# Optimization experiments

Hardware: AMD Instinct MI355X
Metric: run time of the kernel (lower is better)

The kernel has to match this reference:

```python
import jax, jax.numpy as jnp
import numpy as np

B, N, T = 1, 4096, 512
WQ, HK = 32, 128
ATOM_S, ATOM_Z, TOKEN_S, TOKEN_Z = 128, 16, 384, 128
FEAT = 3 + 1 + 128 + 4 * 64  # 388


def _indexing_matrix(K, Wq, Hk):
    # faithful port of get_indexing_matrix: one-hot banded gather matrix [2K, K*h]
    h = Hk // (Wq // 2)
    ar = jnp.arange(2 * K)
    idx = jnp.clip(ar[None, :] - ar[:, None] + h // 2, 0, h + 1)
    idx = idx.reshape(K, 2, 2 * K)[:, 0, :]                 # [K, 2K]
    oh = jax.nn.one_hot(idx, h + 2, dtype=jnp.float32)[..., 1:-1]  # [K, 2K, h]
    return jnp.transpose(oh, (1, 0, 2)).reshape(2 * K, K * h)


def _to_keys(x, M, Wq, Hk):
    b, n, d = x.shape
    k = n // Wq
    x = x.reshape(b, 2 * k, Wq // 2, d)
    return jnp.einsum('bjid,jk->bkid', x, M).reshape(b, k, Hk, d)


def _ln(x, g, b, eps=1e-5):
    m = jnp.mean(x, axis=-1, keepdims=True)
    v = jnp.var(x, axis=-1, keepdims=True)
    return (x - m) * jax.lax.rsqrt(v + eps) * g + b


def setup_inputs() -> dict:
    key = jax.random.key(0)
    ks = jax.random.split(key, 24)
    s = 0.02
    tok_idx = jnp.sort(jax.random.randint(ks[0], (B, N), 0, T), axis=-1)
    return {
        'ref_pos': jax.random.normal(ks[1], (B, N, 3), jnp.float32),
        'ref_charge': jax.random.normal(ks[2], (B, N), jnp.float32),
        'ref_element': jax.random.uniform(ks[3], (B, N, 128), jnp.float32),
        'ref_atom_name_chars': jax.random.uniform(ks[4], (B, N, 4, 64), jnp.float32),
        'atom_pad_mask': jnp.ones((B, N), dtype=bool),
        'ref_space_uid': jnp.sort(jax.random.randint(ks[5], (B, N), 0, 512), axis=-1),
        'atom_to_token': jax.nn.one_hot(tok_idx, T, dtype=jnp.float32),
        's_trunk': jax.random.normal(ks[6], (B, T, TOKEN_S), jnp.float32),
        'z': jax.random.normal(ks[7], (B, T, T, TOKEN_Z), jnp.float32),
        # learned params, stored [in, out] so y = x @ W (+ b)
        'W_feat': jax.random.normal(ks[8], (FEAT, ATOM_S), jnp.float32) * s,
        'b_feat': jnp.zeros((ATOM_S,), jnp.float32),
        'W_pos': jax.random.normal(ks[9], (3, ATOM_Z), jnp.float32) * s,
        'W_dist': jax.random.normal(ks[10], (1, ATOM_Z), jnp.float32) * s,
        'W_mask': jax.random.normal(ks[11], (1, ATOM_Z), jnp.float32) * s,
        'ln_s_g': jnp.ones((TOKEN_S,), jnp.float32),
        'ln_s_b': jnp.zeros((TOKEN_S,), jnp.float32),
        'W_s2c': jax.random.normal(ks[12], (TOKEN_S, ATOM_S), jnp.float32) * s,
        'ln_z_g': jnp.ones((TOKEN_Z,), jnp.float32),
        'ln_z_b': jnp.zeros((TOKEN_Z,), jnp.float32),
        'W_z2p': jax.random.normal(ks[13], (TOKEN_Z, ATOM_Z), jnp.float32) * s,
        'W_cq': jax.random.normal(ks[14], (ATOM_S, ATOM_Z), jnp.float32) * s,
        'W_ck': jax.random.normal(ks[15], (ATOM_S, ATOM_Z), jnp.float32) * s,
        'W_m1': jax.random.normal(ks[16], (ATOM_Z, ATOM_Z), jnp.float32) * s,
        'W_m2': jax.random.normal(ks[17], (ATOM_Z, ATOM_Z), jnp.float32) * s,
        'W_m3': jax.random.normal(ks[18], (ATOM_Z, ATOM_Z), jnp.float32) * s,
    }


def reference(ref_pos, ref_charge, ref_element, ref_atom_name_chars, atom_pad_mask,
              ref_space_uid, atom_to_token, s_trunk, z,
              W_feat, b_feat, W_pos, W_dist, W_mask,
              ln_s_g, ln_s_b, W_s2c, ln_z_g, ln_z_b, W_z2p,
              W_cq, W_ck, W_m1, W_m2, W_m3):
    b, n, _ = ref_pos.shape
    k = n // WQ
    atom_feats = jnp.concatenate(
        [ref_pos, ref_charge[..., None], ref_element,
         ref_atom_name_chars.reshape(b, n, 4 * 64)], axis=-1)
    c = atom_feats @ W_feat + b_feat                       # [B,N,atom_s]
    q = c
    M = _indexing_matrix(k, WQ, HK)
    tk = lambda x: _to_keys(x, M, WQ, HK)

    pos_q = ref_pos.reshape(b, k, WQ, 1, 3)
    pos_k = tk(ref_pos).reshape(b, k, 1, HK, 3)
    d = pos_k - pos_q                                      # [B,K,W,H,3]
    d_norm = 1.0 / (1.0 + jnp.sum(d * d, axis=-1, keepdims=True))

    mq = atom_pad_mask.reshape(b, k, WQ, 1)
    mk = tk(atom_pad_mask[..., None].astype(jnp.float32)).reshape(b, k, 1, HK) > 0.5
    uq = ref_space_uid.reshape(b, k, WQ, 1)
    uk = tk(ref_space_uid[..., None].astype(jnp.float32)).reshape(b, k, 1, HK).astype(ref_space_uid.dtype)
    v = (mq & mk & (uq == uk)).astype(jnp.float32)[..., None]  # [B,K,W,H,1]

    p = (d @ W_pos) * v
    p = p + (d_norm @ W_dist) * v
    p = p + (v @ W_mask) * v

    # structure_prediction branch
    s2c = _ln(s_trunk, ln_s_g, ln_s_b) @ W_s2c             # [B,T,atom_s]
    c = c + jnp.einsum('bnt,btd->bnd', atom_to_token, s2c)
    a2t_q = atom_to_token.reshape(b, k, WQ, -1)            # [B,K,W,T]
    a2t_k = tk(atom_to_token)                              # [B,K,H,T]
    zp = _ln(z, ln_z_g, ln_z_b) @ W_z2p                    # [B,T,T,atom_z]
    tmp = jnp.einsum('bwki,bijd->bwkjd', a2t_q, zp)        # [B,K,W,T,atom_z]
    p = p + jnp.einsum('bwkjd,bwlj->bwkld', tmp, a2t_k)    # [B,K,W,H,atom_z]

    p = p + jax.nn.relu(c).reshape(b, k, WQ, 1, -1) @ W_cq
    p = p + jax.nn.relu(tk(c)).reshape(b, k, 1, HK, -1) @ W_ck

    h1 = jax.nn.relu(p) @ W_m1
    h2 = jax.nn.relu(h1) @ W_m2
    p = p + jax.nn.relu(h2) @ W_m3
    return (q, c, p)
```

## Files before the change

kernel.cpp:

```cpp
#include <hip/hip_runtime.h>

#define N_ATOMS 4096
#define T_TOK   512
#define TOKEN_S 384
#define TOKEN_Z 128

using bfrag = __attribute__((ext_vector_type(8))) short;
using f4    = __attribute__((ext_vector_type(4))) float;

__device__ __forceinline__ short f2bf(float f) {
    unsigned u = __float_as_uint(f);
    unsigned r = u + 0x7FFFu + ((u >> 16) & 1u);
    return (short)(r >> 16);
}
__device__ __forceinline__ float bf2f(unsigned short s) {
    return __uint_as_float(((unsigned)s) << 16);
}

__global__ __launch_bounds__(256) void setup_kernel(
    const float* __restrict__ a2t, const float* __restrict__ Wz,
    const float* __restrict__ gz, const float* __restrict__ bz,
    const float* __restrict__ Wf, const float* __restrict__ Wcq,
    const float* __restrict__ Wck, const float* __restrict__ Ws2c,
    const float* __restrict__ gs, const float* __restrict__ bs,
    int* __restrict__ tok, short* __restrict__ zpW,
    short* __restrict__ featW, short* __restrict__ WcqF,
    short* __restrict__ WckF, short* __restrict__ s2cW,
    float* __restrict__ bias16, float* __restrict__ cs16,
    float* __restrict__ cs128, float* __restrict__ bs128,
    int* __restrict__ lo, int* __restrict__ hi) {
    const int b = blockIdx.x, tid = threadIdx.x;
    if (b >= 53) {
        const int wave = tid >> 6, lane = tid & 63;
        const int n = (b - 53) * 4 + wave;
        const float* row = a2t + (size_t)n * T_TOK;
        int found = 0;
#pragma unroll
        for (int m = 0; m < T_TOK / 64; ++m)
            if (row[lane + 64 * m] > 0.5f) found = lane + 64 * m;
#pragma unroll
        for (int off = 32; off >= 1; off >>= 1)
            found = max(found, __shfl_xor(found, off, 64));
        if (lane == 0) tok[n] = found;
        return;
    }
    if (b == 51) {
        const int o = tid >> 3, s = tid & 7;
        const float* vec = (o < 16) ? bz : gz;
        const int n = o & 15;
        float p = 0.f;
#pragma unroll
        for (int i = 0; i < 16; ++i) {
            const int k = s + 8 * i;
            p += vec[k] * Wz[k * 16 + n];
        }
        p += __shfl_xor(p, 1, 64); p += __shfl_xor(p, 2, 64);
        p += __shfl_xor(p, 4, 64);
        if (s == 0) { if (o < 16) bias16[n] = p; else cs16[n] = p; }
        return;
    }
    if (b == 52) {
        lo[tid] = 0x7FFFFFFF; lo[tid + 256] = 0x7FFFFFFF;
        hi[tid] = -1;         hi[tid + 256] = -1;
        const int o = tid & 127, arr = tid >> 7;
        const float* vec = arr ? bs : gs;
        float s = 0.f;
        for (int k = 0; k < TOKEN_S; ++k)
            s += vec[k] * Ws2c[(size_t)k * 128 + o];
        if (arr) bs128[o] = s; else cs128[o] = s;
        return;
    }
    const int id = b * 256 + tid;
    const int lane = id & 63, fs = id >> 6;
    const int quad = lane >> 4, n = lane & 15;
    short v[8];
    short* dst;
    if (fs < 4) {
#pragma unroll
        for (int j = 0; j < 8; ++j) {
            int k = fs * 32 + quad * 8 + j;
            v[j] = f2bf(gz[k] * Wz[k * 16 + n]);
        }
        dst = zpW + (size_t)(fs * 64 + lane) * 8;
    } else if (fs < 100) {
        const int idx = fs - 4, kb = idx >> 3, nt = idx & 7;
#pragma unroll
        for (int j = 0; j < 8; ++j) {
            int f = 4 + kb * 32 + quad * 8 + j;
            v[j] = f2bf(Wf[(size_t)f * 128 + nt * 16 + n]);
        }
        dst = featW + (size_t)(idx * 64 + lane) * 8;
    } else if (fs < 104) {
        const int kb = fs - 100;
#pragma unroll
        for (int j = 0; j < 8; ++j) {
            int k = kb * 32 + quad * 8 + j;
            v[j] = f2bf(Wcq[k * 16 + n]);
        }
        dst = WcqF + (size_t)(kb * 64 + lane) * 8;
    } else if (fs < 108) {
        const int kb = fs - 104;
#pragma unroll
        for (int j = 0; j < 8; ++j) {
            int k = kb * 32 + quad * 8 + j;
            v[j] = f2bf(Wck[k * 16 + n]);
        }
        dst = WckF + (size_t)(kb * 64 + lane) * 8;
    } else {
        const int idx = fs - 108, kb = idx >> 3, nt = idx & 7;
#pragma unroll
        for (int j = 0; j < 8; ++j) {
            int k = kb * 32 + quad * 8 + j;
            v[j] = f2bf(gs[k] * Ws2c[(size_t)k * 128 + nt * 16 + n]);
        }
        dst = s2cW + (size_t)(idx * 64 + lane) * 8;
    }
#pragma unroll
    for (int j = 0; j < 8; ++j) dst[j] = v[j];
}

__global__ __launch_bounds__(256) void band_kernel(
    const int* __restrict__ tok, int* __restrict__ lo, int* __restrict__ hi) {
    const int a = blockIdx.x * 256 + threadIdx.x;
    const int t = tok[a];
    int am = a - 79; if (am < 0) am = 0;
    int ap = a + 79; if (ap > N_ATOMS - 1) ap = N_ATOMS - 1;
    atomicMin(&lo[t], tok[am]);
    atomicMax(&hi[t], tok[ap]);
}

__global__ __launch_bounds__(512) void worklist_kernel(
    const int* __restrict__ lo, const int* __restrict__ hi,
    int* __restrict__ wl, int* __restrict__ wl_count) {
    __shared__ int scan[512];
    const int t = threadIdx.x;
    const int l = lo[t], h = hi[t];
    const int n = (h >= l) ? ((h - l) >> 4) + 1 : 0;
    scan[t] = n;
    __syncthreads();
    for (int off = 1; off < 512; off <<= 1) {
        int add = (t >= off) ? scan[t - off] : 0;
        __syncthreads();
        scan[t] += add;
        __syncthreads();
    }
    const int off0 = scan[t] - n;
    for (int i = 0; i < n; ++i) {
        int tk0 = l + i * 16;
        if (tk0 > T_TOK - 16) tk0 = T_TOK - 16;
        wl[off0 + i] = (t << 16) | tk0;
    }
    if (t == 511) *wl_count = scan[511];
}

__global__ __launch_bounds__(256) void s2c_mfma_kernel(
    const float* __restrict__ s_trunk, const short* __restrict__ s2cW,
    const float* __restrict__ cs128, const float* __restrict__ bs128,
    float* __restrict__ s2c) {
    const int wave = threadIdx.x >> 6, lane = threadIdx.x & 63;
    const int m = lane & 15, quad = lane >> 4;
    const int wg = blockIdx.x * 4 + wave;
    const int tile = wg >> 3, nt = wg & 7;
    const int t0 = tile * 16;
    const float* xrow = s_trunk + (size_t)(t0 + m) * TOKEN_S;

    bfrag A[12];
    float xs = 0.f, xq = 0.f;
#pragma unroll
    for (int kb = 0; kb < 12; ++kb) {
        const float4* p = (const float4*)(xrow + kb * 32 + quad * 8);
        float4 x0 = p[0], x1 = p[1];
        const float xv[8] = {x0.x, x0.y, x0.z, x0.w, x1.x, x1.y, x1.z, x1.w};
#pragma unroll
        for (int j = 0; j < 8; ++j) {
            A[kb][j] = f2bf(xv[j]);
            xs += xv[j]; xq = fmaf(xv[j], xv[j], xq);
        }
    }
    xs += __shfl_xor(xs, 16, 64); xs += __shfl_xor(xs, 32, 64);
    xq += __shfl_xor(xq, 16, 64); xq += __shfl_xor(xq, 32, 64);
    const float mean = xs * (1.f / TOKEN_S);
    const float var  = xq * (1.f / TOKEN_S) - mean * mean;
    const float rstd = rsqrtf(var + 1e-5f);
    const float mrs  = mean * rstd;

    const bfrag* Bb = (const bfrag*)s2cW;
    f4 acc = {0.f, 0.f, 0.f, 0.f};
#pragma unroll
    for (int kb = 0; kb < 12; ++kb)
        acc = __builtin_amdgcn_mfma_f32_16x16x32_bf16(
            A[kb], Bb[(kb * 8 + nt) * 64 + lane], acc, 0, 0, 0);

    const int cn = nt * 16 + m;
    const float csn = cs128[cn], bsn = bs128[cn];
#pragma unroll
    for (int reg = 0; reg < 4; ++reg) {
        const int r = quad * 4 + reg;
        const float rs = __shfl(rstd, r, 64);
        const float ms = __shfl(mrs, r, 64);
        s2c[(size_t)(t0 + r) * 128 + cn] = rs * acc[reg] - ms * csn + bsn;
    }
}

__global__ __launch_bounds__(256) void zp_wl_kernel(
    const float* __restrict__ z, const short* __restrict__ zpW,
    const float* __restrict__ bias16, const float* __restrict__ cs16,
    const int* __restrict__ wl, const int* __restrict__ wl_count,
    unsigned short* __restrict__ zp_bf) {
    const int wave = threadIdx.x >> 6, lane = threadIdx.x & 63;
    const int m = lane & 15, quad = lane >> 4;
    const int nwaves = gridDim.x * 4;
    const int count = *wl_count;
    const bfrag* wb = (const bfrag*)zpW;
    const float csn = cs16[m], bn = bias16[m];

    for (int idx = blockIdx.x * 4 + wave; idx < count; idx += nwaves) {
        const int e = wl[idx];
        const int tq = e >> 16, tk0 = e & 0xFFFF;
        const size_t r0 = (size_t)tq * T_TOK + tk0;
        const float* zrow = z + (r0 + m) * (size_t)TOKEN_Z;

        bfrag A[4];
        float xs = 0.f, xq = 0.f;
#pragma unroll
        for (int kb = 0; kb < 4; ++kb) {
            const float4* p = (const float4*)(zrow + kb * 32 + quad * 8);
            float4 x0 = p[0], x1 = p[1];
            const float xv[8] = {x0.x, x0.y, x0.z, x0.w,
                                 x1.x, x1.y, x1.z, x1.w};
#pragma unroll
            for (int j = 0; j < 8; ++j) {
                A[kb][j] = f2bf(xv[j]);
                xs += xv[j]; xq = fmaf(xv[j], xv[j], xq);
            }
        }
        xs += __shfl_xor(xs, 16, 64); xs += __shfl_xor(xs, 32, 64);
        xq += __shfl_xor(xq, 16, 64); xq += __shfl_xor(xq, 32, 64);
        const float mean = xs * (1.f / TOKEN_Z);
        const float var  = xq * (1.f / TOKEN_Z) - mean * mean;
        const float rstd = rsqrtf(var + 1e-5f);
        const float mrs  = mean * rstd;

        f4 acc = {0.f, 0.f, 0.f, 0.f};
#pragma unroll
        for (int kb = 0; kb < 4; ++kb)
            acc = __builtin_amdgcn_mfma_f32_16x16x32_bf16(
                A[kb], wb[kb * 64 + lane], acc, 0, 0, 0);
#pragma unroll
        for (int reg = 0; reg < 4; ++reg) {
            const int r = quad * 4 + reg;
            const float rs = __shfl(rstd, r, 64);
            const float ms = __shfl(mrs, r, 64);
            zp_bf[(r0 + r) * 16 + m] =
                (unsigned short)f2bf(rs * acc[reg] - ms * csn + bn);
        }
    }
}

__global__ __launch_bounds__(128) void featcatk_kernel(
    const float* __restrict__ pos, const float* __restrict__ charge,
    const float* __restrict__ elem, const float* __restrict__ namec,
    const float* __restrict__ Wf, const float* __restrict__ bf,
    const float* __restrict__ s2c, const int* __restrict__ tok,
    const short* __restrict__ featW, const short* __restrict__ WcqF,
    const short* __restrict__ WckF, float* __restrict__ q_out,
    float* __restrict__ c_out, float* __restrict__ acq,
    float* __restrict__ ack) {
    __shared__ short ctile[16 * 136];
    const int wave = threadIdx.x >> 6, lane = threadIdx.x & 63;
    const int m = lane & 15, quad = lane >> 4;
    const int a0 = blockIdx.x * 16;
    const int ntb = wave * 4;

    f4 acc[4];
#pragma unroll
    for (int nt = 0; nt < 4; ++nt) acc[nt] = (f4){0.f, 0.f, 0.f, 0.f};
    const bfrag* Bb = (const bfrag*)featW;
#pragma unroll
    for (int kb = 0; kb < 12; ++kb) {
        const int f0 = kb * 32 + quad * 8;
        const float* src = (kb < 4)
            ? (elem + (size_t)(a0 + m) * 128 + f0)
            : (namec + (size_t)(a0 + m) * 256 + f0 - 128);
        float4 x0 = ((const float4*)src)[0];
        float4 x1 = ((const float4*)src)[1];
        bfrag A;
        A[0] = f2bf(x0.x); A[1] = f2bf(x0.y); A[2] = f2bf(x0.z); A[3] = f2bf(x0.w);
        A[4] = f2bf(x1.x); A[5] = f2bf(x1.y); A[6] = f2bf(x1.z); A[7] = f2bf(x1.w);
#pragma unroll
        for (int nt = 0; nt < 4; ++nt)
            acc[nt] = __builtin_amdgcn_mfma_f32_16x16x32_bf16(
                A, Bb[(kb * 8 + ntb + nt) * 64 + lane], acc[nt], 0, 0, 0);
    }
    float px[4], py[4], pz[4], ch[4];
    int tk4[4];
#pragma unroll
    for (int reg = 0; reg < 4; ++reg) {
        const int a = a0 + quad * 4 + reg;
        px[reg] = pos[a * 3 + 0]; py[reg] = pos[a * 3 + 1];
        pz[reg] = pos[a * 3 + 2]; ch[reg] = charge[a];
        tk4[reg] = tok[a];
    }
#pragma unroll
    for (int nt = 0; nt < 4; ++nt) {
        const int cn = (ntb + nt) * 16 + m;
        const float w0 = Wf[cn], w1 = Wf[128 + cn], w2 = Wf[256 + cn],
                    w3 = Wf[384 + cn], bv = bf[cn];
#pragma unroll
        for (int reg = 0; reg < 4; ++reg) {
            const int r = quad * 4 + reg;
            float qv = acc[nt][reg] + px[reg] * w0 + py[reg] * w1 +
                       pz[reg] * w2 + ch[reg] * w3 + bv;
            q_out[(size_t)(a0 + r) * 128 + cn] = qv;
            float cv = qv + s2c[(size_t)tk4[reg] * 128 + cn];
            c_out[(size_t)(a0 + r) * 128 + cn] = cv;
            ctile[r * 136 + cn] = f2bf(fmaxf(cv, 0.f));
        }
    }
    __syncthreads();
    const bfrag* BW = wave ? (const bfrag*)WckF : (const bfrag*)WcqF;
    float* dst = wave ? ack : acq;
    f4 a2 = {0.f, 0.f, 0.f, 0.f};
#pragma unroll
    for (int kb = 0; kb < 4; ++kb) {
        bfrag Af = *(const bfrag*)&ctile[m * 136 + kb * 32 + quad * 8];
        a2 = __builtin_amdgcn_mfma_f32_16x16x32_bf16(Af, BW[kb * 64 + lane],
                                                     a2, 0, 0, 0);
    }
#pragma unroll
    for (int reg = 0; reg < 4; ++reg)
        dst[(size_t)(a0 + quad * 4 + reg) * 16 + m] = a2[reg];
}

__global__ __launch_bounds__(256) void pair_mfma_kernel(
    const float* __restrict__ pos, const int* __restrict__ uid,
    const int* __restrict__ tok, const unsigned short* __restrict__ zp_bf,
    const float* __restrict__ acq, const float* __restrict__ ack,
    const float* __restrict__ W_pos, const float* __restrict__ W_dist,
    const float* __restrict__ W_mask, const float* __restrict__ W_m1,
    const float* __restrict__ W_m2, const float* __restrict__ W_m3,
    float* __restrict__ p_out) {
    const int wave = threadIdx.x >> 6, lane = threadIdx.x & 63;
    const int m = lane & 15, quad = lane >> 4;
    const int qa = blockIdx.x * 4 + wave;
    const int j = qa >> 5;

    bfrag A1, A2, A3;
#pragma unroll
    for (int jj = 0; jj < 4; ++jj) {
        const int d = quad * 4 + jj;
        A1[jj] = f2bf(W_m1[d * 16 + m]); A1[jj + 4] = 0;
        A2[jj] = f2bf(W_m2[d * 16 + m]); A2[jj + 4] = 0;
        A3[jj] = f2bf(W_m3[d * 16 + m]); A3[jj + 4] = 0;
    }
    float wp0[4], wp1[4], wp2[4], wd[4], wm[4];
#pragma unroll
    for (int jj = 0; jj < 4; ++jj) {
        const int d = quad * 4 + jj;
        wp0[jj] = W_pos[d]; wp1[jj] = W_pos[16 + d]; wp2[jj] = W_pos[32 + d];
        wd[jj] = W_dist[d]; wm[jj] = W_mask[d];
    }
    const float pqx = pos[qa * 3 + 0], pqy = pos[qa * 3 + 1],
                pqz = pos[qa * 3 + 2];
    const int uq = uid[qa], tq = tok[qa];
    const float4 aq = *(const float4*)(acq + (size_t)qa * 16 + quad * 4);
    const float aqv[4] = {aq.x, aq.y, aq.z, aq.w};
    float* pbase = p_out + (size_t)qa * 2048;

    const f4 zero = {0.f, 0.f, 0.f, 0.f};
#pragma unroll
    for (int g = 0; g < 8; ++g) {
        const int kk = g * 16 + m;
        const int src = j * 32 + kk - 48;
        const bool valid = ((unsigned)src < (unsigned)N_ATOMS);
        float dx = 0.f, dy = 0.f, dz = 0.f, dn = 0.f, vflag = 0.f;
        float zv[4] = {0.f, 0.f, 0.f, 0.f}, av[4] = {0.f, 0.f, 0.f, 0.f};
        if (valid) {
            dx = pos[src * 3 + 0] - pqx;
            dy = pos[src * 3 + 1] - pqy;
            dz = pos[src * 3 + 2] - pqz;
            dn = 1.f / (1.f + dx * dx + dy * dy + dz * dz);
            vflag = (uid[src] == uq) ? 1.f : 0.f;
            const int tk_ = tok[src];
            ushort4 zl = *(const ushort4*)(zp_bf +
                            ((size_t)tq * T_TOK + tk_) * 16 + quad * 4);
            float4 al = *(const float4*)(ack + (size_t)src * 16 + quad * 4);
            zv[0] = bf2f(zl.x); zv[1] = bf2f(zl.y);
            zv[2] = bf2f(zl.z); zv[3] = bf2f(zl.w);
            av[0] = al.x; av[1] = al.y; av[2] = al.z; av[3] = al.w;
        }
        float pb[4];
        bfrag B;
#pragma unroll
        for (int jj = 0; jj < 4; ++jj) {
            float t = dx * wp0[jj] + dy * wp1[jj] + dz * wp2[jj] +
                      dn * wd[jj] + wm[jj];
            pb[jj] = vflag * t + zv[jj] + av[jj] + aqv[jj];
            B[jj] = f2bf(fmaxf(pb[jj], 0.f));
            B[jj + 4] = 0;
        }
        f4 t1 = __builtin_amdgcn_mfma_f32_16x16x32_bf16(A1, B, zero, 0, 0, 0);
        bfrag B2;
#pragma unroll
        for (int jj = 0; jj < 4; ++jj) {
            B2[jj] = f2bf(fmaxf(t1[jj], 0.f)); B2[jj + 4] = 0;
        }
        f4 t2 = __builtin_amdgcn_mfma_f32_16x16x32_bf16(A2, B2, zero, 0, 0, 0);
        bfrag B3;
#pragma unroll
        for (int jj = 0; jj < 4; ++jj) {
            B3[jj] = f2bf(fmaxf(t2[jj], 0.f)); B3[jj + 4] = 0;
        }
        f4 t3 = __builtin_amdgcn_mfma_f32_16x16x32_bf16(A3, B3, zero, 0, 0, 0);
        float4 o = make_float4(pb[0] + t3[0], pb[1] + t3[1],
                               pb[2] + t3[2], pb[3] + t3[3]);
        *(float4*)(pbase + kk * 16 + quad * 4) = o;
    }
}

extern "C" void kernel_launch(void* const* d_in, const int* in_sizes, int n_in,
                              void* d_out, int out_size, void* d_ws, size_t ws_size,
                              hipStream_t stream) {
    const float* ref_pos     = (const float*)d_in[0];
    const float* ref_charge  = (const float*)d_in[1];
    const float* ref_element = (const float*)d_in[2];
    const float* ref_name    = (const float*)d_in[3];
    const int*   uid         = (const int*)d_in[5];
    const float* a2t         = (const float*)d_in[6];
    const float* s_trunk     = (const float*)d_in[7];
    const float* z           = (const float*)d_in[8];
    const float* W_feat      = (const float*)d_in[9];
    const float* b_feat      = (const float*)d_in[10];
    const float* W_pos       = (const float*)d_in[11];
    const float* W_dist      = (const float*)d_in[12];
    const float* W_mask      = (const float*)d_in[13];
    const float* ln_s_g      = (const float*)d_in[14];
    const float* ln_s_b      = (const float*)d_in[15];
    const float* W_s2c       = (const float*)d_in[16];
    const float* ln_z_g      = (const float*)d_in[17];
    const float* ln_z_b      = (const float*)d_in[18];
    const float* W_z2p       = (const float*)d_in[19];
    const float* W_cq        = (const float*)d_in[20];
    const float* W_ck        = (const float*)d_in[21];
    const float* W_m1        = (const float*)d_in[22];
    const float* W_m2        = (const float*)d_in[23];
    const float* W_m3        = (const float*)d_in[24];

    float* out = (float*)d_out;
    float* q_out = out;
    float* c_out = out + 524288;
    float* p_out = out + 1048576;

    char* w = (char*)d_ws;
    unsigned short* zp_bf = (unsigned short*)w;
    float* s2c  = (float*)(w + 8388608);
    float* acq  = s2c + 65536;
    float* ack  = acq + 65536;
    int*   tok  = (int*)(ack + 65536);
    short* zpW   = (short*)(tok + 4096);
    short* featW = zpW + 2048;
    short* WcqF  = featW + 49152;
    short* WckF  = WcqF + 2048;
    short* s2cW  = WckF + 2048;
    float* bias16 = (float*)(s2cW + 49152);
    float* cs16   = bias16 + 16;
    float* cs128  = cs16 + 16;
    float* bs128  = cs128 + 128;
    int*   lo     = (int*)(bs128 + 128);
    int*   hi     = lo + 512;
    int*   wl     = hi + 512;
    int*   wl_cnt = wl + 16448;

    setup_kernel<<<1077, 256, 0, stream>>>(a2t, W_z2p, ln_z_g, ln_z_b,
                                           W_feat, W_cq, W_ck, W_s2c,
                                           ln_s_g, ln_s_b, tok, zpW, featW,
                                           WcqF, WckF, s2cW, bias16, cs16,
                                           cs128, bs128, lo, hi);
    band_kernel<<<16, 256, 0, stream>>>(tok, lo, hi);
    worklist_kernel<<<1, 512, 0, stream>>>(lo, hi, wl, wl_cnt);
    s2c_mfma_kernel<<<64, 256, 0, stream>>>(s_trunk, s2cW, cs128, bs128, s2c);
    zp_wl_kernel<<<512, 256, 0, stream>>>(z, zpW, bias16, cs16, wl, wl_cnt,
                                          zp_bf);
    featcatk_kernel<<<256, 128, 0, stream>>>(ref_pos, ref_charge, ref_element,
                                             ref_name, W_feat, b_feat, s2c, tok,
                                             featW, WcqF, WckF,
                                             q_out, c_out, acq, ack);
    pair_mfma_kernel<<<1024, 256, 0, stream>>>(ref_pos, uid, tok, zp_bf,
                                               acq, ack, W_pos, W_dist, W_mask,
                                               W_m1, W_m2, W_m3, p_out);
}
```

Measured before the change: 277.7 us.

## Merge band/worklist into s2c kernel and zp into feat kernel to cut launches

Replaces the separate band (global atomics) and worklist kernels with one extra block of the s2c kernel, which builds lo/hi with shared-memory atomics and scans them locally. The zp worklist kernel and the feature/c kernel become one launch split by block index. Seven launches drop to four, which removes launch gaps and lets independent work share one grid. The cost is heterogeneous blocks: a single serial block handles the banding, and the feature blocks now process 32 atoms with 256 threads.

```diff
diff --git a/kernel.cpp b/kernel.cpp
--- a/kernel.cpp
+++ b/kernel.cpp
@@ -27,8 +27,7 @@
     short* __restrict__ featW, short* __restrict__ WcqF,
     short* __restrict__ WckF, short* __restrict__ s2cW,
     float* __restrict__ bias16, float* __restrict__ cs16,
-    float* __restrict__ cs128, float* __restrict__ bs128,
-    int* __restrict__ lo, int* __restrict__ hi) {
+    float* __restrict__ cs128, float* __restrict__ bs128) {
     const int b = blockIdx.x, tid = threadIdx.x;
     if (b >= 53) {
         const int wave = tid >> 6, lane = tid & 63;
@@ -60,8 +59,6 @@
         return;
     }
     if (b == 52) {
-        lo[tid] = 0x7FFFFFFF; lo[tid + 256] = 0x7FFFFFFF;
-        hi[tid] = -1;         hi[tid + 256] = -1;
         const int o = tid & 127, arr = tid >> 7;
         const float* vec = arr ? bs : gs;
         float s = 0.f;
@@ -119,49 +116,50 @@
     for (int j = 0; j < 8; ++j) dst[j] = v[j];
 }
 
-__global__ __launch_bounds__(256) void band_kernel(
-    const int* __restrict__ tok, int* __restrict__ lo, int* __restrict__ hi) {
-    const int a = blockIdx.x * 256 + threadIdx.x;
-    const int t = tok[a];
-    int am = a - 79; if (am < 0) am = 0;
-    int ap = a + 79; if (ap > N_ATOMS - 1) ap = N_ATOMS - 1;
-    atomicMin(&lo[t], tok[am]);
-    atomicMax(&hi[t], tok[ap]);
-}
-
-__global__ __launch_bounds__(512) void worklist_kernel(
-    const int* __restrict__ lo, const int* __restrict__ hi,
-    int* __restrict__ wl, int* __restrict__ wl_count) {
-    __shared__ int scan[512];
-    const int t = threadIdx.x;
-    const int l = lo[t], h = hi[t];
-    const int n = (h >= l) ? ((h - l) >> 4) + 1 : 0;
-    scan[t] = n;
-    __syncthreads();
-    for (int off = 1; off < 512; off <<= 1) {
-        int add = (t >= off) ? scan[t - off] : 0;
-        __syncthreads();
-        scan[t] += add;
-        __syncthreads();
-    }
-    const int off0 = scan[t] - n;
-    for (int i = 0; i < n; ++i) {
-        int tk0 = l + i * 16;
-        if (tk0 > T_TOK - 16) tk0 = T_TOK - 16;
-        wl[off0 + i] = (t << 16) | tk0;
-    }
-    if (t == 511) *wl_count = scan[511];
-}
-
-__global__ __launch_bounds__(256) void s2c_mfma_kernel(
+__global__ __launch_bounds__(512) void s2c_band_kernel(
     const float* __restrict__ s_trunk, const short* __restrict__ s2cW,
     const float* __restrict__ cs128, const float* __restrict__ bs128,
-    float* __restrict__ s2c) {
+    const int* __restrict__ tok, float* __restrict__ s2c,
+    int* __restrict__ wl, int* __restrict__ wl_count) {
+    __shared__ int sh_lo[512], sh_hi[512], scan[512];
+    const int b = blockIdx.x;
+    if (b == 32) {
+        const int t = threadIdx.x;
+        sh_lo[t] = 0x7FFFFFFF; sh_hi[t] = -1;
+        __syncthreads();
+#pragma unroll
+        for (int i = 0; i < 8; ++i) {
+            const int a = t * 8 + i;
+            const int tt = tok[a];
+            int am = a - 79; if (am < 0) am = 0;
+            int ap = a + 79; if (ap > N_ATOMS - 1) ap = N_ATOMS - 1;
+            atomicMin(&sh_lo[tt], tok[am]);
+            atomicMax(&sh_hi[tt], tok[ap]);
+        }
+        __syncthreads();
+        const int l = sh_lo[t], h = sh_hi[t];
+        const int n = (h >= l) ? ((h - l) >> 4) + 1 : 0;
+        scan[t] = n;
+        __syncthreads();
+        for (int off = 1; off < 512; off <<= 1) {
+            int add = (t >= off) ? scan[t - off] : 0;
+            __syncthreads();
+            scan[t] += add;
+            __syncthreads();
+        }
+        const int off0 = scan[t] - n;
+        for (int i = 0; i < n; ++i) {
+            int tk0 = l + i * 16;
+            if (tk0 > T_TOK - 16) tk0 = T_TOK - 16;
+            wl[off0 + i] = (t << 16) | tk0;
+        }
+        if (t == 511) *wl_count = scan[511];
+        return;
+    }
     const int wave = threadIdx.x >> 6, lane = threadIdx.x & 63;
     const int m = lane & 15, quad = lane >> 4;
-    const int wg = blockIdx.x * 4 + wave;
-    const int tile = wg >> 3, nt = wg & 7;
-    const int t0 = tile * 16;
+    const int nt = wave;
+    const int t0 = b * 16;
     const float* xrow = s_trunk + (size_t)(t0 + m) * TOKEN_S;
 
     bfrag A[12];
@@ -202,62 +200,11 @@
     }
 }
 
-__global__ __launch_bounds__(256) void zp_wl_kernel(
+__global__ __launch_bounds__(256) void zp_feat_kernel(
     const float* __restrict__ z, const short* __restrict__ zpW,
     const float* __restrict__ bias16, const float* __restrict__ cs16,
     const int* __restrict__ wl, const int* __restrict__ wl_count,
-    unsigned short* __restrict__ zp_bf) {
-    const int wave = threadIdx.x >> 6, lane = threadIdx.x & 63;
-    const int m = lane & 15, quad = lane >> 4;
-    const int nwaves = gridDim.x * 4;
-    const int count = *wl_count;
-    const bfrag* wb = (const bfrag*)zpW;
-    const float csn = cs16[m], bn = bias16[m];
-
-    for (int idx = blockIdx.x * 4 + wave; idx < count; idx += nwaves) {
-        const int e = wl[idx];
-        const int tq = e >> 16, tk0 = e & 0xFFFF;
-        const size_t r0 = (size_t)tq * T_TOK + tk0;
-        const float* zrow = z + (r0 + m) * (size_t)TOKEN_Z;
-
-        bfrag A[4];
-        float xs = 0.f, xq = 0.f;
-#pragma unroll
-        for (int kb = 0; kb < 4; ++kb) {
-            const float4* p = (const float4*)(zrow + kb * 32 + quad * 8);
-            float4 x0 = p[0], x1 = p[1];
-            const float xv[8] = {x0.x, x0.y, x0.z, x0.w,
-                                 x1.x, x1.y, x1.z, x1.w};
-#pragma unroll
-            for (int j = 0; j < 8; ++j) {
-                A[kb][j] = f2bf(xv[j]);
-                xs += xv[j]; xq = fmaf(xv[j], xv[j], xq);
-            }
-        }
-        xs += __shfl_xor(xs, 16, 64); xs += __shfl_xor(xs, 32, 64);
-        xq += __shfl_xor(xq, 16, 64); xq += __shfl_xor(xq, 32, 64);
-        const float mean = xs * (1.f / TOKEN_Z);
-        const float var  = xq * (1.f / TOKEN_Z) - mean * mean;
-        const float rstd = rsqrtf(var + 1e-5f);
-        const float mrs  = mean * rstd;
-
-        f4 acc = {0.f, 0.f, 0.f, 0.f};
-#pragma unroll
-        for (int kb = 0; kb < 4; ++kb)
-            acc = __builtin_amdgcn_mfma_f32_16x16x32_bf16(
-                A[kb], wb[kb * 64 + lane], acc, 0, 0, 0);
-#pragma unroll
-        for (int reg = 0; reg < 4; ++reg) {
-            const int r = quad * 4 + reg;
-            const float rs = __shfl(rstd, r, 64);
-            const float ms = __shfl(mrs, r, 64);
-            zp_bf[(r0 + r) * 16 + m] =
-                (unsigned short)f2bf(rs * acc[reg] - ms * csn + bn);
-        }
-    }
-}
-
-__global__ __launch_bounds__(128) void featcatk_kernel(
+    unsigned short* __restrict__ zp_bf,
     const float* __restrict__ pos, const float* __restrict__ charge,
     const float* __restrict__ elem, const float* __restrict__ namec,
     const float* __restrict__ Wf, const float* __restrict__ bf,
@@ -266,11 +213,62 @@
     const short* __restrict__ WckF, float* __restrict__ q_out,
     float* __restrict__ c_out, float* __restrict__ acq,
     float* __restrict__ ack) {
-    __shared__ short ctile[16 * 136];
+    __shared__ short ctile[32 * 136];
     const int wave = threadIdx.x >> 6, lane = threadIdx.x & 63;
     const int m = lane & 15, quad = lane >> 4;
-    const int a0 = blockIdx.x * 16;
-    const int ntb = wave * 4;
+
+    if (blockIdx.x < 512) {
+        const int count = *wl_count;
+        const bfrag* wb = (const bfrag*)zpW;
+        const float csn = cs16[m], bn = bias16[m];
+
+        for (int idx = blockIdx.x * 4 + wave; idx < count; idx += 2048) {
+            const int e = wl[idx];
+            const int tq = e >> 16, tk0 = e & 0xFFFF;
+            const size_t r0 = (size_t)tq * T_TOK + tk0;
+            const float* zrow = z + (r0 + m) * (size_t)TOKEN_Z;
+
+            bfrag A[4];
+            float xs = 0.f, xq = 0.f;
+#pragma unroll
+            for (int kb = 0; kb < 4; ++kb) {
+                const float4* p = (const float4*)(zrow + kb * 32 + quad * 8);
+                float4 x0 = p[0], x1 = p[1];
+                const float xv[8] = {x0.x, x0.y, x0.z, x0.w,
+                                     x1.x, x1.y, x1.z, x1.w};
+#pragma unroll
+                for (int j = 0; j < 8; ++j) {
+                    A[kb][j] = f2bf(xv[j]);
+                    xs += xv[j]; xq = fmaf(xv[j], xv[j], xq);
+                }
+            }
+            xs += __shfl_xor(xs, 16, 64); xs += __shfl_xor(xs, 32, 64);
+            xq += __shfl_xor(xq, 16, 64); xq += __shfl_xor(xq, 32, 64);
+            const float mean = xs * (1.f / TOKEN_Z);
+            const float var  = xq * (1.f / TOKEN_Z) - mean * mean;
+            const float rstd = rsqrtf(var + 1e-5f);
+            const float mrs  = mean * rstd;
+
+            f4 acc = {0.f, 0.f, 0.f, 0.f};
+#pragma unroll
+            for (int kb = 0; kb < 4; ++kb)
+                acc = __builtin_amdgcn_mfma_f32_16x16x32_bf16(
+                    A[kb], wb[kb * 64 + lane], acc, 0, 0, 0);
+#pragma unroll
+            for (int reg = 0; reg < 4; ++reg) {
+                const int r = quad * 4 + reg;
+                const float rs = __shfl(rstd, r, 64);
+                const float ms = __shfl(mrs, r, 64);
+                zp_bf[(r0 + r) * 16 + m] =
+                    (unsigned short)f2bf(rs * acc[reg] - ms * csn + bn);
+            }
+        }
+        return;
+    }
+
+    const int sub = wave >> 1, w2 = wave & 1;
+    const int a0 = (blockIdx.x - 512) * 32 + sub * 16;
+    const int ntb = w2 * 4;
 
     f4 acc[4];
 #pragma unroll
@@ -304,26 +302,26 @@
 #pragma unroll
     for (int nt = 0; nt < 4; ++nt) {
         const int cn = (ntb + nt) * 16 + m;
-        const float w0 = Wf[cn], w1 = Wf[128 + cn], w2 = Wf[256 + cn],
+        const float w0 = Wf[cn], w1 = Wf[128 + cn], w2f = Wf[256 + cn],
                     w3 = Wf[384 + cn], bv = bf[cn];
 #pragma unroll
         for (int reg = 0; reg < 4; ++reg) {
             const int r = quad * 4 + reg;
             float qv = acc[nt][reg] + px[reg] * w0 + py[reg] * w1 +
-                       pz[reg] * w2 + ch[reg] * w3 + bv;
+                       pz[reg] * w2f + ch[reg] * w3 + bv;
             q_out[(size_t)(a0 + r) * 128 + cn] = qv;
             float cv = qv + s2c[(size_t)tk4[reg] * 128 + cn];
             c_out[(size_t)(a0 + r) * 128 + cn] = cv;
-            ctile[r * 136 + cn] = f2bf(fmaxf(cv, 0.f));
+            ctile[(sub * 16 + r) * 136 + cn] = f2bf(fmaxf(cv, 0.f));
         }
     }
     __syncthreads();
-    const bfrag* BW = wave ? (const bfrag*)WckF : (const bfrag*)WcqF;
-    float* dst = wave ? ack : acq;
+    const bfrag* BW = w2 ? (const bfrag*)WckF : (const bfrag*)WcqF;
+    float* dst = w2 ? ack : acq;
     f4 a2 = {0.f, 0.f, 0.f, 0.f};
 #pragma unroll
     for (int kb = 0; kb < 4; ++kb) {
-        bfrag Af = *(const bfrag*)&ctile[m * 136 + kb * 32 + quad * 8];
+        bfrag Af = *(const bfrag*)&ctile[(sub * 16 + m) * 136 + kb * 32 + quad * 8];
         a2 = __builtin_amdgcn_mfma_f32_16x16x32_bf16(Af, BW[kb * 64 + lane],
                                                      a2, 0, 0, 0);
     }
@@ -466,25 +464,22 @@
     float* cs16   = bias16 + 16;
     float* cs128  = cs16 + 16;
     float* bs128  = cs128 + 128;
-    int*   lo     = (int*)(bs128 + 128);
-    int*   hi     = lo + 512;
-    int*   wl     = hi + 512;
+    int*   wl     = (int*)(bs128 + 128);
     int*   wl_cnt = wl + 16448;
 
     setup_kernel<<<1077, 256, 0, stream>>>(a2t, W_z2p, ln_z_g, ln_z_b,
                                            W_feat, W_cq, W_ck, W_s2c,
                                            ln_s_g, ln_s_b, tok, zpW, featW,
                                            WcqF, WckF, s2cW, bias16, cs16,
-                                           cs128, bs128, lo, hi);
-    band_kernel<<<16, 256, 0, stream>>>(tok, lo, hi);
-    worklist_kernel<<<1, 512, 0, stream>>>(lo, hi, wl, wl_cnt);
-    s2c_mfma_kernel<<<64, 256, 0, stream>>>(s_trunk, s2cW, cs128, bs128, s2c);
-    zp_wl_kernel<<<512, 256, 0, stream>>>(z, zpW, bias16, cs16, wl, wl_cnt,
-                                          zp_bf);
-    featcatk_kernel<<<256, 128, 0, stream>>>(ref_pos, ref_charge, ref_element,
-                                             ref_name, W_feat, b_feat, s2c, tok,
-                                             featW, WcqF, WckF,
-                                             q_out, c_out, acq, ack);
+                                           cs128, bs128);
+    s2c_band_kernel<<<33, 512, 0, stream>>>(s_trunk, s2cW, cs128, bs128,
+                                            tok, s2c, wl, wl_cnt);
+    zp_feat_kernel<<<640, 256, 0, stream>>>(z, zpW, bias16, cs16, wl, wl_cnt,
+                                            zp_bf,
+                                            ref_pos, ref_charge, ref_element,
+                                            ref_name, W_feat, b_feat, s2c, tok,
+                                            featW, WcqF, WckF,
+                                            q_out, c_out, acq, ack);
     pair_mfma_kernel<<<1024, 256, 0, stream>>>(ref_pos, uid, tok, zp_bf,
                                                acq, ack, W_pos, W_dist, W_mask,
                                                W_m1, W_m2, W_m3, p_out);
```

After: 263.8 us. 1.05x faster.
